# Kernel tuning notes

Hardware: AMD Instinct MI355X
Metric: run time of the kernel (lower is better)

Reference implementation:

```python
import jax, jax.numpy as jnp
import numpy as np
from jax import lax

INPUT_SIZE = 512
THRESHOLD = 0.5
IOU_TH = 0.3
MAX_ROIS = 32   # py_cpu_nms(...)[:32]
ROI = 7
NEG = jnp.float32(-1e30)


def _make_anchors(fh, fw, stride):
    # 3 scales x 3 ratios = 9 anchors per cell, laid out in (h, w, anchor)
    # order to match permute(0,2,3,1).view(-1) of the conv heads.
    scales = np.array([32.0, 64.0, 128.0])
    ratios = np.array([0.5, 1.0, 2.0])
    ws = (scales[:, None] * np.sqrt(ratios)[None, :]).reshape(-1)
    hs = (scales[:, None] / np.sqrt(ratios)[None, :]).reshape(-1)
    cy = (np.arange(fh) + 0.5) * stride
    cx = (np.arange(fw) + 0.5) * stride
    CX, CY = np.meshgrid(cx, cy)
    CX = CX[..., None]; CY = CY[..., None]
    a = np.stack([CX - ws / 2, CY - hs / 2, CX + ws / 2, CY + hs / 2], axis=-1)
    return jnp.asarray(a.reshape(-1, 4), jnp.float32)


def setup_inputs() -> dict:
    key = jax.random.key(0)
    k1, k2, k3 = jax.random.split(key, 3)
    B, C, FH, FW, A, stride = 4, 256, 64, 64, 9, 8
    featureMap = jax.random.normal(k1, (B, C, FH, FW), jnp.float32)
    # small init so sigmoid scores spread across threshold and exp(tw) stays sane
    w_cls = jax.random.normal(k2, (A, C, 3, 3), jnp.float32) * 0.05
    w_loc = jax.random.normal(k3, (4 * A, C, 3, 3), jnp.float32) * 0.01
    prior_anchor = _make_anchors(FH, FW, stride)
    return {"featureMap": featureMap, "prior_anchor": prior_anchor,
            "w_cls": w_cls, "w_loc": w_loc, "stride": stride}


def _conv(x, w):
    return lax.conv_general_dilated(x, w, (1, 1), "SAME",
                                    dimension_numbers=("NCHW", "OIHW", "NCHW"))


def _decode(loc, anchors):
    aw = anchors[:, 2] - anchors[:, 0]
    ah = anchors[:, 3] - anchors[:, 1]
    acx = anchors[:, 0] + 0.5 * aw
    acy = anchors[:, 1] + 0.5 * ah
    cx = acx + loc[:, 0] * aw
    cy = acy + loc[:, 1] * ah
    w = aw * jnp.exp(loc[:, 2])
    h = ah * jnp.exp(loc[:, 3])
    return jnp.stack([cx - 0.5 * w, cy - 0.5 * h, cx + 0.5 * w, cy + 0.5 * h], axis=1)


def _iou_one(box, boxes):
    xx1 = jnp.maximum(box[0], boxes[:, 0]); yy1 = jnp.maximum(box[1], boxes[:, 1])
    xx2 = jnp.minimum(box[2], boxes[:, 2]); yy2 = jnp.minimum(box[3], boxes[:, 3])
    inter = jnp.clip(xx2 - xx1, 0) * jnp.clip(yy2 - yy1, 0)
    a1 = (box[2] - box[0]) * (box[3] - box[1])
    a2 = (boxes[:, 2] - boxes[:, 0]) * (boxes[:, 3] - boxes[:, 1])
    return inter / (a1 + a2 - inter + 1e-9)


def _nms(boxes, scores, valid):
    # greedy NMS, fixed MAX_ROIS rounds (== sort-by-score py_cpu_nms + [:32])
    N = scores.shape[0]
    s0 = jnp.where(valid, scores, -1.0)

    def body(i, carry):
        s, picks, ok = carry
        idx = jnp.argmax(s)
        good = s[idx] > 0.0
        picks = picks.at[i].set(idx.astype(jnp.int32))
        ok = ok.at[i].set(good)
        sup = (_iou_one(boxes[idx], boxes) > IOU_TH) | (jnp.arange(N) == idx)
        return (jnp.where(sup, -1.0, s), picks, ok)

    _, picks, ok = lax.fori_loop(
        0, MAX_ROIS, body,
        (s0, jnp.zeros(MAX_ROIS, jnp.int32), jnp.zeros(MAX_ROIS, bool)))
    return picks, ok


def _ceil_div(a, b):
    return -(-a // b)


def _adaptive_maxpool(feat, box):
    # feat: [C, FH, FW]; box: int32 [x1, y1, x2, y2] in feature-map coords.
    # Faithful F.adaptive_max_pool2d bins: start=floor(i*h/7), end=ceil((i+1)*h/7).
    FH, FW = feat.shape[1], feat.shape[2]
    x1, y1, x2, y2 = box[0], box[1], box[2], box[3]
    h = y2 - y1; w = x2 - x1
    i = jnp.arange(ROI)
    rs = y1 + (i * h) // ROI; re = y1 + _ceil_div((i + 1) * h, ROI)
    cs = x1 + (i * w) // ROI; ce = x1 + _ceil_div((i + 1) * w, ROI)
    hh = jnp.arange(FH); ww = jnp.arange(FW)
    rm = jnp.where((hh >= rs[:, None]) & (hh < re[:, None]), 0.0, NEG)  # [7, FH]
    cm = jnp.where((ww >= cs[:, None]) & (ww < ce[:, None]), 0.0, NEG)  # [7, FW]
    t = jnp.max(feat[None] + rm[:, None, :, None], axis=2)              # [7, C, FW]
    out = jnp.max(t[:, None] + cm[None, :, None, :], axis=3)            # [7, 7, C]
    return jnp.transpose(out, (2, 0, 1))                                # [C, 7, 7]


def reference(featureMap, prior_anchor, w_cls, w_loc, stride):
    B, C, FH, FW = featureMap.shape
    cls = jax.nn.sigmoid(_conv(featureMap, w_cls))                      # [B, A, FH, FW]
    cls = jnp.transpose(cls, (0, 2, 3, 1)).reshape(B, -1)               # [B, N]
    loc = jnp.transpose(_conv(featureMap, w_loc), (0, 2, 3, 1)).reshape(B, -1, 4)
    boxes = jax.vmap(_decode, in_axes=(0, None))(loc, prior_anchor)     # [B, N, 4]
    boxes = jnp.clip(boxes, 0.0, float(INPUT_SIZE))                     # clamp(0, input_size)
    valid = (cls > THRESHOLD) \
          & (boxes[..., 2] - boxes[..., 0] >= 2 * stride) \
          & (boxes[..., 3] - boxes[..., 1] >= 2 * stride)
    picks, ok = jax.vmap(_nms)(boxes, cls, valid)                       # [B, 32]
    sel_boxes = jnp.take_along_axis(boxes, picks[..., None], axis=1)    # [B, 32, 4]
    sel_scores = jnp.take_along_axis(cls, picks, axis=1)                # [B, 32]
    eval_boxes = jnp.where(
        ok[..., None],
        jnp.concatenate([sel_boxes, sel_scores[..., None]], axis=-1), 0.0)
    # src_coordinate.int() / stride -> integer feature-map coords
    ib = sel_boxes.astype(jnp.int32) // stride
    fx1 = jnp.clip(ib[..., 0], 0, FW - 1); fy1 = jnp.clip(ib[..., 1], 0, FH - 1)
    fx2 = jnp.clip(ib[..., 2], fx1 + 1, FW); fy2 = jnp.clip(ib[..., 3], fy1 + 1, FH)
    fb = jnp.stack([fx1, fy1, fx2, fy2], axis=-1).reshape(-1, 4)        # [B*32, 4]
    img = jnp.repeat(jnp.arange(B), MAX_ROIS)
    rois = lax.map(lambda a: _adaptive_maxpool(featureMap[a[1]], a[0]), (fb, img))
    rois = jnp.where(ok.reshape(-1)[:, None, None, None], rois, 0.0)    # [B*32, 256, 7, 7]
    return eval_boxes, ok, rois
```

## Files before the change

kernel.cpp:

```cpp
#include <hip/hip_runtime.h>
#include <hip/hip_bf16.h>

#define FHH 64
#define FWW 64
#define CIN 256
#define NB 4
#define NA 9
#define NANCH 36864
#define NPOS 4096
#define OC_TOTAL 45
#define OCP 48
#define MAXROIS 32
#define ROI 7
#define NEGV -1e30f
#define NCHUNK 576
#define NTH 16
#define CAP 1024

typedef unsigned long long u64;

__device__ __constant__ const float TH_LADDER[NTH] = {
    0.9999f, 0.9998f, 0.9995f, 0.999f, 0.998f, 0.997f, 0.995f, 0.993f,
    0.99f, 0.987f, 0.984f, 0.98f, 0.975f, 0.97f, 0.96f, 0.0f};

__device__ __forceinline__ void pick_threshold(
    const int* __restrict__ gcnt, int b, int cap,
    float* T, int* C, int* V, int* frc)
{
    int bestc = 0; float bt = TH_LADDER[0];
#pragma unroll
    for (int i = 0; i < NTH; ++i) {
        int c = gcnt[b * NTH + i];
        if (c <= cap && c > bestc) { bestc = c; bt = TH_LADDER[i]; }
    }
    int f = (gcnt[b * NTH + 0] > cap) ? 1 : 0;
    if (f) { bestc = cap; bt = TH_LADDER[0]; }
    *T = bt; *C = bestc; *V = gcnt[b * NTH + NTH - 1]; *frc = f;
}

__global__ __launch_bounds__(256) void wtrans_kernel(
    const float* __restrict__ wcls,
    const float* __restrict__ wloc,
    float* __restrict__ wT,
    int* __restrict__ gcnt)
{
    if (blockIdx.x == 0 && threadIdx.x < NB * NTH) gcnt[threadIdx.x] = 0;
    int idx = blockIdx.x * 256 + threadIdx.x;
    int o = idx % 48;
    int rest = idx / 48;
    int tap = rest % 9;
    int c = rest / 9;
    float v = 0.f;
    if (o < OC_TOTAL) {
        v = (o < NA) ? wcls[((size_t)o * CIN + c) * 9 + tap]
                     : wloc[((size_t)(o - NA) * CIN + c) * 9 + tap];
    }
    wT[idx] = v;
}

__global__ __launch_bounds__(256) void conv_kernel(
    const float* __restrict__ feat,
    const float* __restrict__ wT,
    float* __restrict__ partial,
    int nkg, int cpk)
{
    __shared__ float flds[16][18][20];

    int blk = blockIdx.x;
    int low = blk & 7;
    int rest = blk >> 3;
    int kg = rest % nkg;
    int uhi = rest / nkg;
    int unit = uhi * 8 + low;
    int b = unit >> 4;
    int tile = unit & 15;

    int ty0 = (tile >> 2) * 16;
    int tx0 = (tile & 3) * 16;

    int pb = threadIdx.x & 63;
    int q = __builtin_amdgcn_readfirstlane(threadIdx.x >> 6);
    int ry0 = (pb >> 3) * 2;
    int rx0 = (pb & 7) * 2;

    int cbase = kg * cpk;

    float acc[2][2][12];
#pragma unroll
    for (int py = 0; py < 2; ++py)
#pragma unroll
        for (int px = 0; px < 2; ++px)
#pragma unroll
            for (int o = 0; o < 12; ++o) acc[py][px][o] = 0.f;

    for (int c0 = 0; c0 < cpk; c0 += 16) {
        __syncthreads();
        for (int idx = threadIdx.x; idx < 16 * 324; idx += 256) {
            int c = idx / 324;
            int r = idx - c * 324;
            int y = r / 18;
            int x = r - y * 18;
            int gy = ty0 + y - 1;
            int gx = tx0 + x - 1;
            float v = 0.f;
            if ((unsigned)gy < FHH && (unsigned)gx < FWW)
                v = feat[((size_t)(b * CIN + cbase + c0 + c) * FHH + gy) * FWW + gx];
            flds[c][y][x] = v;
        }
        __syncthreads();

        const float* wq = wT + (size_t)(cbase + c0) * 432 + q * 12;
        for (int c = 0; c < 16; ++c) {
            float f[4][4];
#pragma unroll
            for (int r = 0; r < 4; ++r) {
                float2 a0 = *(const float2*)&flds[c][ry0 + r][rx0];
                float2 a1 = *(const float2*)&flds[c][ry0 + r][rx0 + 2];
                f[r][0] = a0.x; f[r][1] = a0.y; f[r][2] = a1.x; f[r][3] = a1.y;
            }
#pragma unroll
            for (int tap = 0; tap < 9; ++tap) {
                int dy = tap / 3, dx = tap % 3;
                const float* wp = wq + (c * 9 + tap) * 48;
                float w[12];
#pragma unroll
                for (int o = 0; o < 12; ++o) w[o] = wp[o];
#pragma unroll
                for (int py = 0; py < 2; ++py)
#pragma unroll
                for (int px = 0; px < 2; ++px) {
                    float fv = f[py + dy][px + dx];
#pragma unroll
                    for (int o = 0; o < 12; ++o)
                        acc[py][px][o] += fv * w[o];
                }
            }
        }
    }

    float* pout = partial + ((size_t)kg * NB + b) * OCP * NPOS;
#pragma unroll
    for (int o = 0; o < 12; ++o) {
        int oo = q * 12 + o;
        if (oo >= OC_TOTAL) continue;
        float* op = pout + (size_t)oo * NPOS;
#pragma unroll
        for (int py = 0; py < 2; ++py)
#pragma unroll
        for (int px = 0; px < 2; ++px) {
            int pos = (ty0 + ry0 + py) * FWW + (tx0 + rx0 + px);
            op[pos] = acc[py][px][o];
        }
    }
}

__global__ __launch_bounds__(256) void decode_kernel(
    const float* __restrict__ partial,
    const float* __restrict__ anchors,
    const int* __restrict__ stridep,
    float* __restrict__ boxes,
    float* __restrict__ scores,
    int* __restrict__ gcnt,
    int* __restrict__ gcount,
    int nkg)
{
    __shared__ int hcnt[NTH];
    if (threadIdx.x < NTH) hcnt[threadIdx.x] = 0;
    if (blockIdx.x == 0 && threadIdx.x < NB) gcount[threadIdx.x] = 0;
    __syncthreads();

    int t = blockIdx.x * 256 + threadIdx.x;
    int pos = t & (NPOS - 1);
    int ba = t >> 12;
    int b = ba / 9;
    int a = ba - b * 9;

    float cls = 0.f, l0 = 0.f, l1 = 0.f, l2 = 0.f, l3 = 0.f;
    for (int kg = 0; kg < nkg; ++kg) {
        const float* pk = partial + ((size_t)kg * NB + b) * OCP * NPOS;
        cls += pk[(size_t)a * NPOS + pos];
        l0 += pk[(size_t)(NA + a * 4 + 0) * NPOS + pos];
        l1 += pk[(size_t)(NA + a * 4 + 1) * NPOS + pos];
        l2 += pk[(size_t)(NA + a * 4 + 2) * NPOS + pos];
        l3 += pk[(size_t)(NA + a * 4 + 3) * NPOS + pos];
    }

    float sig = 1.f / (1.f + expf(-cls));
    int n = pos * NA + a;
    const float* an = anchors + (size_t)n * 4;
    float ax1 = an[0], ay1 = an[1], ax2 = an[2], ay2 = an[3];
    float aw = ax2 - ax1, ah = ay2 - ay1;
    float acx = ax1 + 0.5f * aw, acy = ay1 + 0.5f * ah;
    float cx = acx + l0 * aw;
    float cy = acy + l1 * ah;
    float w = aw * expf(l2);
    float h = ah * expf(l3);
    float x1 = fminf(fmaxf(cx - 0.5f * w, 0.f), 512.f);
    float y1 = fminf(fmaxf(cy - 0.5f * h, 0.f), 512.f);
    float x2 = fminf(fmaxf(cx + 0.5f * w, 0.f), 512.f);
    float y2 = fminf(fmaxf(cy + 0.5f * h, 0.f), 512.f);
    int stride = stridep[0];
    float msz = 2.f * (float)stride;
    bool valid = (sig > 0.5f) && ((x2 - x1) >= msz) && ((y2 - y1) >= msz);
    ((float4*)boxes)[(size_t)b * NANCH + n] = make_float4(x1, y1, x2, y2);
    scores[(size_t)b * NANCH + n] = valid ? sig : -1.0f;

#pragma unroll
    for (int i = 0; i < NTH; ++i) {
        u64 mb = __ballot(valid && sig >= TH_LADDER[i]);
        if ((threadIdx.x & 63) == 0 && mb)
            atomicAdd(&hcnt[i], (int)__popcll(mb));
    }
    __syncthreads();
    if (threadIdx.x < NTH && hcnt[threadIdx.x])
        atomicAdd(&gcnt[b * NTH + threadIdx.x], hcnt[threadIdx.x]);
}

__global__ __launch_bounds__(256) void nms_compact_kernel(
    const float* __restrict__ scores,
    const int* __restrict__ gcnt,
    int* __restrict__ gcount,
    u64* __restrict__ candkey,
    int cap)
{
    __shared__ int lcnt;
    __shared__ int wbase[4];
    __shared__ int gbase;
    int t = blockIdx.x * 256 + threadIdx.x;
    int b = t / NANCH;
    int j = t - b * NANCH;
    int lane = threadIdx.x & 63;
    int w = threadIdx.x >> 6;
    if (threadIdx.x == 0) lcnt = 0;
    __syncthreads();

    float T; int C, V, frc;
    pick_threshold(gcnt, b, cap, &T, &C, &V, &frc);

    float v = scores[t];
    bool p = (v > 0.f) && (v >= T);
    u64 m = __ballot(p);
    int cnt = (int)__popcll(m);
    if (lane == 0) wbase[w] = atomicAdd(&lcnt, cnt);
    __syncthreads();
    if (threadIdx.x == 0) gbase = lcnt ? atomicAdd(&gcount[b], lcnt) : 0;
    __syncthreads();
    if (p) {
        int off = (int)__popcll(m & ((1ULL << lane) - 1ULL));
        int slot = gbase + wbase[w] + off;
        if (slot < cap)
            candkey[(size_t)b * cap + slot] =
                ((u64)__float_as_uint(v) << 32) | (unsigned int)(~j);
    }
}

__device__ __forceinline__ void write_outputs(
    int b, int i, bool okv, int idx, float sc,
    const float4* Bb4, const int* stridep,
    float* d_out, int* ifb, int* iok)
{
    float4 bb = Bb4[idx];
    float* eb = d_out + ((size_t)b * MAXROIS + i) * 5;
    eb[0] = okv ? bb.x : 0.f;
    eb[1] = okv ? bb.y : 0.f;
    eb[2] = okv ? bb.z : 0.f;
    eb[3] = okv ? bb.w : 0.f;
    eb[4] = okv ? sc : 0.f;
    d_out[NB * MAXROIS * 5 + b * MAXROIS + i] = okv ? 1.f : 0.f;
    int st = stridep[0];
    int fx1 = min(max(((int)bb.x) / st, 0), FWW - 1);
    int fy1 = min(max(((int)bb.y) / st, 0), FHH - 1);
    int fx2 = min(max(((int)bb.z) / st, fx1 + 1), FWW);
    int fy2 = min(max(((int)bb.w) / st, fy1 + 1), FHH);
    int r = b * MAXROIS + i;
    ifb[r * 4 + 0] = fx1;
    ifb[r * 4 + 1] = fy1;
    ifb[r * 4 + 2] = fx2;
    ifb[r * 4 + 3] = fy2;
    iok[r] = okv ? 1 : 0;
}

__global__ __launch_bounds__(512) void nms_sortscan_kernel(
    const u64* __restrict__ candkey,
    const float* __restrict__ boxes,
    const int* __restrict__ gcnt,
    const int* __restrict__ stridep,
    float* __restrict__ d_out,
    int* __restrict__ ifb, int* __restrict__ iok, int* __restrict__ flag,
    int cap)
{
    __shared__ u64 skey[CAP];
    __shared__ float4 box_l[CAP];
    __shared__ u64 mask[CAP / 64];
    __shared__ int picks[MAXROIS];
    __shared__ int np_sh;

    int b = blockIdx.x;
    int tid = threadIdx.x;
    int lane = tid & 63;
    if (tid == 0) np_sh = 0;

    float T; int C, V, frc;
    pick_threshold(gcnt, b, cap, &T, &C, &V, &frc);

    int CSZ = 64;
    while (CSZ < C) CSZ <<= 1;

    for (int j = tid; j < CSZ; j += 512)
        skey[j] = (j < C) ? candkey[(size_t)b * cap + j] : 0ULL;

    int prev_cross = 1;
    for (int kk = 2; kk <= CSZ; kk <<= 1) {
        for (int jj = kk >> 1; jj > 0; jj >>= 1) {
            int cross = (jj >= 128) ? 1 : 0;
            if (cross || prev_cross) __syncthreads();
            for (int tt = tid; tt < (CSZ >> 1); tt += 512) {
                int i = ((tt & ~(jj - 1)) << 1) | (tt & (jj - 1));
                int l = i + jj;
                u64 a = skey[i], c2 = skey[l];
                bool up = ((i & kk) == 0);
                bool sw = up ? (a < c2) : (a > c2);
                if (sw) { skey[i] = c2; skey[l] = a; }
            }
            prev_cross = cross;
        }
    }
    __syncthreads();

    const float4* Bb4 = (const float4*)(boxes + (size_t)b * NANCH * 4);
    for (int j = tid; j < C; j += 512) {
        int id = (int)(~((unsigned int)(skey[j] & 0xFFFFFFFFULL)));
        box_l[j] = Bb4[id];
    }
    if (tid < CAP / 64) {
        int base = tid * 64;
        u64 m0;
        if (base >= C) m0 = ~0ULL;
        else if (base + 64 > C) m0 = ~((1ULL << (C - base)) - 1ULL);
        else m0 = 0ULL;
        mask[tid] = m0;
    }
    __syncthreads();

    for (int round = 0; round < MAXROIS; ++round) {
        u64 mw = (lane < CAP / 64) ? mask[lane] : ~0ULL;
        int bpos = __ffsll((u64)(~mw));
        int cand = bpos ? lane * 64 + bpos - 1 : 0x7FFFFFFF;
#pragma unroll
        for (int off = 32; off >= 1; off >>= 1)
            cand = min(cand, __shfl_xor(cand, off));
        int pj = cand;
        if (pj == 0x7FFFFFFF) break;
        if (tid == 0) {
            picks[round] = pj;
            np_sh = round + 1;
            atomicOr(&mask[pj >> 6], 1ULL << (pj & 63));
        }
        float4 pb = box_l[pj];
        float parea = (pb.z - pb.x) * (pb.w - pb.y);
        int j0 = tid * 2;
        u64 curm = mask[tid >> 5];
        u64 addm = 0ULL;
#pragma unroll
        for (int d = 0; d < 2; ++d) {
            int j = j0 + d;
            if (j > pj && j < C && !((curm >> (j & 63)) & 1ULL)) {
                float4 bb2 = box_l[j];
                float xx1 = fmaxf(pb.x, bb2.x), yy1 = fmaxf(pb.y, bb2.y);
                float xx2 = fminf(pb.z, bb2.z), yy2 = fminf(pb.w, bb2.w);
                float inter = fmaxf(xx2 - xx1, 0.f) * fmaxf(yy2 - yy1, 0.f);
                float a2 = (bb2.z - bb2.x) * (bb2.w - bb2.y);
                float iou = inter / (parea + a2 - inter + 1e-9f);
                if (iou > 0.3f) addm |= 1ULL << (j & 63);
            }
        }
        if (addm) atomicOr(&mask[tid >> 5], addm);
        __syncthreads();
    }
    __syncthreads();

    int np = np_sh;
    bool need_fb = frc || (np < MAXROIS && V > C);
    if (tid == 0) flag[b] = need_fb ? 1 : 0;
    if (!need_fb && tid < MAXROIS) {
        int i = tid;
        bool okv = i < np;
        int slot = okv ? picks[i] : 0;
        u64 k = skey[slot];
        int idx = okv ? (int)(~((unsigned int)(k & 0xFFFFFFFFULL))) : 0;
        float sc = okv ? __uint_as_float((unsigned int)(k >> 32)) : 0.f;
        write_outputs(b, i, okv, idx, sc, Bb4, stridep, d_out, ifb, iok);
    }
}

__global__ __launch_bounds__(1024) void nms_fallback_kernel(
    const float* __restrict__ boxes,
    const float* __restrict__ scores,
    const int* __restrict__ stridep,
    float* __restrict__ d_out,
    int* __restrict__ ifb,
    int* __restrict__ iok,
    const int* __restrict__ flag)
{
    __shared__ float s[NANCH];
    __shared__ float2 cmax[NCHUNK];
    __shared__ int   picks_sh[MAXROIS];
    __shared__ float pscore_sh[MAXROIS];

    int b = blockIdx.x;
    if (flag[b] == 0) return;

    const float4* Bb4 = (const float4*)(boxes + (size_t)b * NANCH * 4);
    const float* Sb = scores + (size_t)b * NANCH;
    int lane = threadIdx.x & 63;
    int w = threadIdx.x >> 6;

    for (int k = 0; k < 36; ++k) {
        int ch = w * 36 + k;
        int j = ch * 64 + lane;
        float v = Sb[j];
        s[j] = v;
        float bv = v; int bi = j;
#pragma unroll
        for (int off = 32; off >= 1; off >>= 1) {
            float ov = __shfl_xor(bv, off);
            int   oi = __shfl_xor(bi, off);
            if (ov > bv || (ov == bv && oi < bi)) { bv = ov; bi = oi; }
        }
        if (lane == 0) cmax[ch] = make_float2(bv, __int_as_float(bi));
    }
    __syncthreads();
    if (w != 0) return;

    float px1 = 0.f, py1 = 0.f, px2 = 0.f, py2 = 0.f, parea = 0.f;
    int np = 0;
    while (np < MAXROIS) {
        float bv = -2.f; int bi = 0x7fffffff;
#pragma unroll
        for (int k = 0; k < 9; ++k) {
            float2 cm = cmax[lane * 9 + k];
            int ci = __float_as_int(cm.y);
            if (cm.x > bv || (cm.x == bv && ci < bi)) { bv = cm.x; bi = ci; }
        }
#pragma unroll
        for (int off = 32; off >= 1; off >>= 1) {
            float ov = __shfl_xor(bv, off);
            int   oi = __shfl_xor(bi, off);
            if (ov > bv || (ov == bv && oi < bi)) { bv = ov; bi = oi; }
        }
        if (bv <= 0.f) break;
        int fi = bi; float fs = bv;

        float4 cbb = Bb4[fi];

        bool sup = false;
        if (lane < np) {
            float xx1 = fmaxf(px1, cbb.x), yy1 = fmaxf(py1, cbb.y);
            float xx2 = fminf(px2, cbb.z), yy2 = fminf(py2, cbb.w);
            float inter = fmaxf(xx2 - xx1, 0.f) * fmaxf(yy2 - yy1, 0.f);
            float a2 = (cbb.z - cbb.x) * (cbb.w - cbb.y);
            float iou = inter / (parea + a2 - inter + 1e-9f);
            sup = iou > 0.3f;
        }
        u64 m = __ballot(sup);

        int ch = fi >> 6;
        int j = ch * 64 + lane;
        float sv = (j == fi) ? -1.f : s[j];
        if (j == fi) s[j] = -1.f;
        float nv = sv; int ni = j;
#pragma unroll
        for (int off = 32; off >= 1; off >>= 1) {
            float ov = __shfl_xor(nv, off);
            int   oi = __shfl_xor(ni, off);
            if (ov > nv || (ov == nv && oi < ni)) { nv = ov; ni = oi; }
        }
        if (lane == 0) cmax[ch] = make_float2(nv, __int_as_float(ni));

        if (m == 0ULL) {
            if (lane == np) {
                px1 = cbb.x; py1 = cbb.y; px2 = cbb.z; py2 = cbb.w;
                parea = (px2 - px1) * (py2 - py1);
            }
            picks_sh[np] = fi;
            pscore_sh[np] = fs;
            ++np;
        }
    }

    if (lane < MAXROIS) {
        int i = lane;
        bool okv = i < np;
        int idx = okv ? picks_sh[i] : 0;
        float sc = okv ? pscore_sh[i] : 0.f;
        write_outputs(b, i, okv, idx, sc, Bb4, stridep, d_out, ifb, iok);
    }
}

__global__ __launch_bounds__(256) void roi_kernel(
    const float* __restrict__ feat,
    const int* __restrict__ ifb,
    const int* __restrict__ iok,
    float* __restrict__ out_rois)
{
    __shared__ float plane[NPOS];
    __shared__ int sifb[MAXROIS * 4];
    __shared__ int siok[MAXROIS];

    int bc = blockIdx.x;
    int b = bc >> 8;
    int c = bc & 255;

    const float4* F4 = (const float4*)(feat + (size_t)bc * NPOS);
    float4* P4 = (float4*)plane;
    for (int i = threadIdx.x; i < NPOS / 4; i += 256)
        P4[i] = F4[i];
    if (threadIdx.x < MAXROIS * 4) sifb[threadIdx.x] = ifb[b * MAXROIS * 4 + threadIdx.x];
    if (threadIdx.x < MAXROIS) siok[threadIdx.x] = iok[b * MAXROIS + threadIdx.x];
    __syncthreads();

    for (int t = threadIdx.x; t < MAXROIS * 49; t += 256) {
        int r = t / 49;
        int bin = t - r * 49;
        int i = bin / 7;
        int j = bin - i * 7;
        float outv = 0.f;
        if (siok[r]) {
            int x1 = sifb[r * 4 + 0];
            int y1 = sifb[r * 4 + 1];
            int x2 = sifb[r * 4 + 2];
            int y2 = sifb[r * 4 + 3];
            int h = y2 - y1;
            int w = x2 - x1;
            int rs = y1 + (i * h) / ROI;
            int re = y1 + ((i + 1) * h + ROI - 1) / ROI;
            int cs = x1 + (j * w) / ROI;
            int ce = x1 + ((j + 1) * w + ROI - 1) / ROI;
            float m = NEGV;
            for (int y = rs; y < re; ++y) {
                const float* row = plane + y * FWW;
                for (int x = cs; x < ce; ++x) m = fmaxf(m, row[x]);
            }
            outv = m;
        }
        out_rois[((size_t)(b * MAXROIS + r) * CIN + c) * 49 + bin] = outv;
    }
}

extern "C" void kernel_launch(void* const* d_in, const int* in_sizes, int n_in,
                              void* d_out, int out_size, void* d_ws, size_t ws_size,
                              hipStream_t stream) {
    const float* feat    = (const float*)d_in[0];
    const float* anchors = (const float*)d_in[1];
    const float* wcls    = (const float*)d_in[2];
    const float* wloc    = (const float*)d_in[3];
    const int*   stridep = (const int*)d_in[4];
    float* out = (float*)d_out;
    float* ws  = (float*)d_ws;

    const size_t P1 = (size_t)NB * OCP * NPOS;
    const size_t WTN = 256 * 9 * 48;
    const int cap = CAP;

    auto need = [&](int nk) -> size_t {
        size_t f = P1 * nk
                 + 589824 + 147456 + WTN
                 + (size_t)NB * cap * 2
                 + 2048;
        return f * 4;
    };
    int nkg = 16;
    if (ws_size < need(16)) {
        if (ws_size >= need(8)) { nkg = 8; }
        else { nkg = 4; }
    }

    float* partial   = ws;
    float* boxes     = partial + P1 * nkg;
    float* scores    = boxes + (size_t)NB * NANCH * 4;
    float* wT        = scores + (size_t)NB * NANCH;
    u64*   candkey   = (u64*)(wT + WTN);
    float* tailf     = (float*)(candkey + (size_t)NB * cap);
    int*   ifb       = (int*)tailf;
    int*   iok       = ifb + 512;
    int*   flag      = iok + 128;
    int*   gcnt      = flag + 4;
    int*   gcount    = gcnt + 64;

    wtrans_kernel<<<432, 256, 0, stream>>>(wcls, wloc, wT, gcnt);
    conv_kernel<<<64 * nkg, 256, 0, stream>>>(feat, wT, partial, nkg, CIN / nkg);
    decode_kernel<<<(NB * NANCH) / 256, 256, 0, stream>>>(partial, anchors, stridep, boxes, scores, gcnt, gcount, nkg);
    nms_compact_kernel<<<(NB * NANCH) / 256, 256, 0, stream>>>(scores, gcnt, gcount, candkey, cap);
    nms_sortscan_kernel<<<NB, 512, 0, stream>>>(candkey, boxes, gcnt, stridep, out, ifb, iok, flag, cap);
    nms_fallback_kernel<<<NB, 1024, 0, stream>>>(boxes, scores, stridep, out, ifb, iok, flag);
    roi_kernel<<<NB * CIN, 256, 0, stream>>>(feat, ifb, iok, out + NB * MAXROIS * 5 + NB * MAXROIS);
}
```

Baseline: 137.6 us.

## Bucket NMS candidates during decode and halve conv tile width for more blocks

Decode now assigns each valid anchor to an exclusive score bucket and scatters its sort key straight into per-bucket buffers. This removes the separate compaction kernel and the full rescan of scores, and the sort kernel gathers keys from the cumulative buckets. Separately, the conv tile shrinks to 16x8 with one output column per thread, doubling the block count to raise occupancy at the cost of more halo loads and fewer outputs per weight load. The bucket buffers enlarge workspace use, and in-block atomics replace the ballot counting.

```diff
diff --git a/kernel.cpp b/kernel.cpp
--- a/kernel.cpp
+++ b/kernel.cpp
@@ -23,19 +23,19 @@
     0.9999f, 0.9998f, 0.9995f, 0.999f, 0.998f, 0.997f, 0.995f, 0.993f,
     0.99f, 0.987f, 0.984f, 0.98f, 0.975f, 0.97f, 0.96f, 0.0f};
 
-__device__ __forceinline__ void pick_threshold(
+__device__ __forceinline__ void pick_threshold2(
     const int* __restrict__ gcnt, int b, int cap,
-    float* T, int* C, int* V, int* frc)
-{
-    int bestc = 0; float bt = TH_LADDER[0];
+    int* isel, int* C, int* V, int* frc)
+{
+    int cum = 0, bestC = 0, best_i = -1;
 #pragma unroll
     for (int i = 0; i < NTH; ++i) {
-        int c = gcnt[b * NTH + i];
-        if (c <= cap && c > bestc) { bestc = c; bt = TH_LADDER[i]; }
+        cum += gcnt[b * NTH + i];
+        if (cum <= cap && cum > bestC) { bestC = cum; best_i = i; }
     }
     int f = (gcnt[b * NTH + 0] > cap) ? 1 : 0;
-    if (f) { bestc = cap; bt = TH_LADDER[0]; }
-    *T = bt; *C = bestc; *V = gcnt[b * NTH + NTH - 1]; *frc = f;
+    if (f) { bestC = cap; best_i = 0; }
+    *isel = best_i; *C = bestC; *V = cum; *frc = f;
 }
 
 __global__ __launch_bounds__(256) void wtrans_kernel(
@@ -64,7 +64,7 @@
     float* __restrict__ partial,
     int nkg, int cpk)
 {
-    __shared__ float flds[16][18][20];
+    __shared__ float flds[16][18][12];
 
     int blk = blockIdx.x;
     int low = blk & 7;
@@ -72,34 +72,31 @@
     int kg = rest % nkg;
     int uhi = rest / nkg;
     int unit = uhi * 8 + low;
-    int b = unit >> 4;
-    int tile = unit & 15;
-
-    int ty0 = (tile >> 2) * 16;
-    int tx0 = (tile & 3) * 16;
+    int b = unit >> 5;
+    int tile = unit & 31;
+    int ty0 = (tile >> 3) * 16;
+    int tx0 = (tile & 7) * 8;
 
     int pb = threadIdx.x & 63;
     int q = __builtin_amdgcn_readfirstlane(threadIdx.x >> 6);
     int ry0 = (pb >> 3) * 2;
-    int rx0 = (pb & 7) * 2;
+    int rx0 = pb & 7;
 
     int cbase = kg * cpk;
 
-    float acc[2][2][12];
+    float acc[2][12];
 #pragma unroll
     for (int py = 0; py < 2; ++py)
 #pragma unroll
-        for (int px = 0; px < 2; ++px)
-#pragma unroll
-            for (int o = 0; o < 12; ++o) acc[py][px][o] = 0.f;
+        for (int o = 0; o < 12; ++o) acc[py][o] = 0.f;
 
     for (int c0 = 0; c0 < cpk; c0 += 16) {
         __syncthreads();
-        for (int idx = threadIdx.x; idx < 16 * 324; idx += 256) {
-            int c = idx / 324;
-            int r = idx - c * 324;
-            int y = r / 18;
-            int x = r - y * 18;
+        for (int idx = threadIdx.x; idx < 16 * 180; idx += 256) {
+            int c = idx / 180;
+            int r = idx - c * 180;
+            int y = r / 10;
+            int x = r - y * 10;
             int gy = ty0 + y - 1;
             int gx = tx0 + x - 1;
             float v = 0.f;
@@ -111,13 +108,12 @@
 
         const float* wq = wT + (size_t)(cbase + c0) * 432 + q * 12;
         for (int c = 0; c < 16; ++c) {
-            float f[4][4];
-#pragma unroll
-            for (int r = 0; r < 4; ++r) {
-                float2 a0 = *(const float2*)&flds[c][ry0 + r][rx0];
-                float2 a1 = *(const float2*)&flds[c][ry0 + r][rx0 + 2];
-                f[r][0] = a0.x; f[r][1] = a0.y; f[r][2] = a1.x; f[r][3] = a1.y;
-            }
+            float f[4][3];
+#pragma unroll
+            for (int r = 0; r < 4; ++r)
+#pragma unroll
+                for (int k = 0; k < 3; ++k)
+                    f[r][k] = flds[c][ry0 + r][rx0 + k];
 #pragma unroll
             for (int tap = 0; tap < 9; ++tap) {
                 int dy = tap / 3, dx = tap % 3;
@@ -126,13 +122,11 @@
 #pragma unroll
                 for (int o = 0; o < 12; ++o) w[o] = wp[o];
 #pragma unroll
-                for (int py = 0; py < 2; ++py)
-#pragma unroll
-                for (int px = 0; px < 2; ++px) {
-                    float fv = f[py + dy][px + dx];
+                for (int py = 0; py < 2; ++py) {
+                    float fv = f[py + dy][dx];
 #pragma unroll
                     for (int o = 0; o < 12; ++o)
-                        acc[py][px][o] += fv * w[o];
+                        acc[py][o] += fv * w[o];
                 }
             }
         }
@@ -145,11 +139,9 @@
         if (oo >= OC_TOTAL) continue;
         float* op = pout + (size_t)oo * NPOS;
 #pragma unroll
-        for (int py = 0; py < 2; ++py)
-#pragma unroll
-        for (int px = 0; px < 2; ++px) {
-            int pos = (ty0 + ry0 + py) * FWW + (tx0 + rx0 + px);
-            op[pos] = acc[py][px][o];
+        for (int py = 0; py < 2; ++py) {
+            int pos = (ty0 + ry0 + py) * FWW + (tx0 + rx0);
+            op[pos] = acc[py][o];
         }
     }
 }
@@ -161,12 +153,12 @@
     float* __restrict__ boxes,
     float* __restrict__ scores,
     int* __restrict__ gcnt,
-    int* __restrict__ gcount,
+    u64* __restrict__ bucketbuf,
     int nkg)
 {
-    __shared__ int hcnt[NTH];
-    if (threadIdx.x < NTH) hcnt[threadIdx.x] = 0;
-    if (blockIdx.x == 0 && threadIdx.x < NB) gcount[threadIdx.x] = 0;
+    __shared__ int bcnt[NTH];
+    __shared__ int gbs[NTH];
+    if (threadIdx.x < NTH) bcnt[threadIdx.x] = 0;
     __syncthreads();
 
     int t = blockIdx.x * 256 + threadIdx.x;
@@ -205,52 +197,24 @@
     ((float4*)boxes)[(size_t)b * NANCH + n] = make_float4(x1, y1, x2, y2);
     scores[(size_t)b * NANCH + n] = valid ? sig : -1.0f;
 
-#pragma unroll
-    for (int i = 0; i < NTH; ++i) {
-        u64 mb = __ballot(valid && sig >= TH_LADDER[i]);
-        if ((threadIdx.x & 63) == 0 && mb)
-            atomicAdd(&hcnt[i], (int)__popcll(mb));
-    }
-    __syncthreads();
-    if (threadIdx.x < NTH && hcnt[threadIdx.x])
-        atomicAdd(&gcnt[b * NTH + threadIdx.x], hcnt[threadIdx.x]);
-}
-
-__global__ __launch_bounds__(256) void nms_compact_kernel(
-    const float* __restrict__ scores,
-    const int* __restrict__ gcnt,
-    int* __restrict__ gcount,
-    u64* __restrict__ candkey,
-    int cap)
-{
-    __shared__ int lcnt;
-    __shared__ int wbase[4];
-    __shared__ int gbase;
-    int t = blockIdx.x * 256 + threadIdx.x;
-    int b = t / NANCH;
-    int j = t - b * NANCH;
-    int lane = threadIdx.x & 63;
-    int w = threadIdx.x >> 6;
-    if (threadIdx.x == 0) lcnt = 0;
-    __syncthreads();
-
-    float T; int C, V, frc;
-    pick_threshold(gcnt, b, cap, &T, &C, &V, &frc);
-
-    float v = scores[t];
-    bool p = (v > 0.f) && (v >= T);
-    u64 m = __ballot(p);
-    int cnt = (int)__popcll(m);
-    if (lane == 0) wbase[w] = atomicAdd(&lcnt, cnt);
-    __syncthreads();
-    if (threadIdx.x == 0) gbase = lcnt ? atomicAdd(&gcount[b], lcnt) : 0;
-    __syncthreads();
-    if (p) {
-        int off = (int)__popcll(m & ((1ULL << lane) - 1ULL));
-        int slot = gbase + wbase[w] + off;
-        if (slot < cap)
-            candkey[(size_t)b * cap + slot] =
-                ((u64)__float_as_uint(v) << 32) | (unsigned int)(~j);
+    int ib = -1, rloc = 0;
+    if (valid) {
+#pragma unroll
+        for (int i = 0; i < NTH; ++i) {
+            if (sig >= TH_LADDER[i]) { ib = i; break; }
+        }
+        rloc = atomicAdd(&bcnt[ib], 1);
+    }
+    __syncthreads();
+    if (threadIdx.x < NTH)
+        gbs[threadIdx.x] = bcnt[threadIdx.x]
+            ? atomicAdd(&gcnt[b * NTH + threadIdx.x], bcnt[threadIdx.x]) : 0;
+    __syncthreads();
+    if (valid) {
+        int slot = gbs[ib] + rloc;
+        if (slot < CAP)
+            bucketbuf[((size_t)b * NTH + ib) * CAP + slot] =
+                ((u64)__float_as_uint(sig) << 32) | (unsigned int)(~n);
     }
 }
 
@@ -281,13 +245,12 @@
 }
 
 __global__ __launch_bounds__(512) void nms_sortscan_kernel(
-    const u64* __restrict__ candkey,
+    const u64* __restrict__ bucketbuf,
     const float* __restrict__ boxes,
     const int* __restrict__ gcnt,
     const int* __restrict__ stridep,
     float* __restrict__ d_out,
-    int* __restrict__ ifb, int* __restrict__ iok, int* __restrict__ flag,
-    int cap)
+    int* __restrict__ ifb, int* __restrict__ iok, int* __restrict__ flag)
 {
     __shared__ u64 skey[CAP];
     __shared__ float4 box_l[CAP];
@@ -300,14 +263,22 @@
     int lane = tid & 63;
     if (tid == 0) np_sh = 0;
 
-    float T; int C, V, frc;
-    pick_threshold(gcnt, b, cap, &T, &C, &V, &frc);
+    int isel, C, V, frc;
+    pick_threshold2(gcnt, b, CAP, &isel, &C, &V, &frc);
+
+    int off = 0;
+    for (int i = 0; i <= isel; ++i) {
+        int ci = gcnt[b * NTH + i];
+        if (ci > CAP) ci = CAP;
+        for (int j = tid; j < ci; j += 512)
+            skey[off + j] = bucketbuf[((size_t)b * NTH + i) * CAP + j];
+        off += ci;
+        if (off >= CAP) break;
+    }
 
     int CSZ = 64;
     while (CSZ < C) CSZ <<= 1;
-
-    for (int j = tid; j < CSZ; j += 512)
-        skey[j] = (j < C) ? candkey[(size_t)b * cap + j] : 0ULL;
+    for (int j = C + tid; j < CSZ; j += 512) skey[j] = 0ULL;
 
     int prev_cross = 1;
     for (int kk = 2; kk <= CSZ; kk <<= 1) {
@@ -347,8 +318,8 @@
         int bpos = __ffsll((u64)(~mw));
         int cand = bpos ? lane * 64 + bpos - 1 : 0x7FFFFFFF;
 #pragma unroll
-        for (int off = 32; off >= 1; off >>= 1)
-            cand = min(cand, __shfl_xor(cand, off));
+        for (int off2 = 32; off2 >= 1; off2 >>= 1)
+            cand = min(cand, __shfl_xor(cand, off2));
         int pj = cand;
         if (pj == 0x7FFFFFFF) break;
         if (tid == 0) {
@@ -560,12 +531,12 @@
 
     const size_t P1 = (size_t)NB * OCP * NPOS;
     const size_t WTN = 256 * 9 * 48;
-    const int cap = CAP;
+    const size_t BKT = (size_t)NB * NTH * CAP * 2;
 
     auto need = [&](int nk) -> size_t {
         size_t f = P1 * nk
                  + 589824 + 147456 + WTN
-                 + (size_t)NB * cap * 2
+                 + BKT
                  + 2048;
         return f * 4;
     };
@@ -579,19 +550,17 @@
     float* boxes     = partial + P1 * nkg;
     float* scores    = boxes + (size_t)NB * NANCH * 4;
     float* wT        = scores + (size_t)NB * NANCH;
-    u64*   candkey   = (u64*)(wT + WTN);
-    float* tailf     = (float*)(candkey + (size_t)NB * cap);
+    u64*   bucketbuf = (u64*)(wT + WTN);
+    float* tailf     = (float*)(bucketbuf + (size_t)NB * NTH * CAP);
     int*   ifb       = (int*)tailf;
     int*   iok       = ifb + 512;
     int*   flag      = iok + 128;
     int*   gcnt      = flag + 4;
-    int*   gcount    = gcnt + 64;
 
     wtrans_kernel<<<432, 256, 0, stream>>>(wcls, wloc, wT, gcnt);
-    conv_kernel<<<64 * nkg, 256, 0, stream>>>(feat, wT, partial, nkg, CIN / nkg);
-    decode_kernel<<<(NB * NANCH) / 256, 256, 0, stream>>>(partial, anchors, stridep, boxes, scores, gcnt, gcount, nkg);
-    nms_compact_kernel<<<(NB * NANCH) / 256, 256, 0, stream>>>(scores, gcnt, gcount, candkey, cap);
-    nms_sortscan_kernel<<<NB, 512, 0, stream>>>(candkey, boxes, gcnt, stridep, out, ifb, iok, flag, cap);
+    conv_kernel<<<128 * nkg, 256, 0, stream>>>(feat, wT, partial, nkg, CIN / nkg);
+    decode_kernel<<<(NB * NANCH) / 256, 256, 0, stream>>>(partial, anchors, stridep, boxes, scores, gcnt, bucketbuf, nkg);
+    nms_sortscan_kernel<<<NB, 512, 0, stream>>>(bucketbuf, boxes, gcnt, stridep, out, ifb, iok, flag);
     nms_fallback_kernel<<<NB, 1024, 0, stream>>>(boxes, scores, stridep, out, ifb, iok, flag);
     roi_kernel<<<NB * CIN, 256, 0, stream>>>(feat, ifb, iok, out + NB * MAXROIS * 5 + NB * MAXROIS);
 }
```

New measurement: 137.8 us. No clear change (+0.1%).
